# Kernel optimization log

Measured on AMD Instinct MI355X. Metric: run time of the kernel, lower is better.

## Reference

```python
import jax, jax.numpy as jnp
import numpy as np

B, T, D = 4096, 200, 64
H1, H2 = 64, 32


def _prelu(x, a):
    # PReLU with a single learnable slope (torch default num_parameters=1)
    return jnp.where(x >= 0, x, a * x)


def setup_inputs() -> dict:
    key = jax.random.key(0)
    ks = jax.random.split(key, 10)
    behavior = jax.random.normal(ks[0], (B, T, D), dtype=jnp.float32)
    candidate = jax.random.normal(ks[1], (B, D), dtype=jnp.float32)
    mask = jax.random.randint(ks[2], (B, T), 0, 2) > 0
    in_dim = 4 * D
    W1 = jax.random.normal(ks[3], (in_dim, H1), dtype=jnp.float32) / np.sqrt(in_dim)
    b1 = jnp.zeros((H1,), dtype=jnp.float32)
    a1 = jnp.full((1,), 0.25, dtype=jnp.float32)  # torch PReLU default init
    W2 = jax.random.normal(ks[4], (H1, H2), dtype=jnp.float32) / np.sqrt(H1)
    b2 = jnp.zeros((H2,), dtype=jnp.float32)
    a2 = jnp.full((1,), 0.25, dtype=jnp.float32)
    W3 = jax.random.normal(ks[5], (H2, 1), dtype=jnp.float32) / np.sqrt(H2)
    b3 = jnp.zeros((1,), dtype=jnp.float32)
    return {"behavior": behavior, "candidate": candidate, "mask": mask,
            "W1": W1, "b1": b1, "a1": a1,
            "W2": W2, "b2": b2, "a2": a2,
            "W3": W3, "b3": b3}


def reference(behavior, candidate, mask, W1, b1, a1, W2, b2, a2, W3, b3):
    # behavior: [B,T,D], candidate: [B,D], mask: [B,T] bool
    cand = candidate[:, None, :]                       # [B,1,D]
    cand_exp = jnp.broadcast_to(cand, behavior.shape)  # [B,T,D]
    diff = behavior - cand_exp
    prod = behavior * cand_exp
    att_input = jnp.concatenate([behavior, cand_exp, diff, prod], axis=-1)  # [B,T,4D]
    h = _prelu(att_input @ W1 + b1, a1)
    h = _prelu(h @ W2 + b2, a2)
    logits = (h @ W3 + b3)[..., 0]                     # [B,T]
    logits = jnp.where(mask, logits, -jnp.inf)
    w = jax.nn.softmax(logits, axis=-1)                # [B,T]
    user_interest = jnp.einsum('bt,btd->bd', w, behavior)  # [B,D]
    return user_interest
```

## Files before the change

### kernel.cpp

```cpp
#include <hip/hip_runtime.h>
#include <hip/hip_bf16.h>

#define T_LEN 200
#define MT    13

typedef __bf16 bf16x8 __attribute__((ext_vector_type(8)));
typedef __bf16 bf16x4 __attribute__((ext_vector_type(4)));
typedef float  f32x4  __attribute__((ext_vector_type(4)));

#if __has_builtin(__builtin_amdgcn_mfma_f32_16x16x16_bf16)
#define MFMA16(a, b, c) __builtin_amdgcn_mfma_f32_16x16x16_bf16((a), (b), (c), 0, 0, 0)
#elif __has_builtin(__builtin_amdgcn_mfma_f32_16x16x16bf16_1k)
#define MFMA16(a, b, c) __builtin_amdgcn_mfma_f32_16x16x16bf16_1k((a), (b), (c), 0, 0, 0)
#else
static __device__ __forceinline__ f32x4 mfma16_asm(bf16x4 a, bf16x4 b, f32x4 c) {
  asm("v_mfma_f32_16x16x16_bf16 %0, %1, %2, %0" : "+v"(c) : "v"(a), "v"(b));
  return c;
}
#define MFMA16(a, b, c) mfma16_asm((a), (b), (c))
#endif

#define MFMA32(a, b, c) __builtin_amdgcn_mfma_f32_16x16x32_bf16((a), (b), (c), 0, 0, 0)

struct __align__(16) Smem {
  unsigned char w1ac[64 * 144];
  unsigned char w1d [64 * 144];
  float wdiff[64][64];
  float candL[4][64];
};

__device__ __forceinline__ void loadA(const float* __restrict__ behB, int t, int kb,
                                      f32x4* x) {
  if (t < T_LEN) {
    const float* p = behB + (size_t)t * 64 + kb;
    x[0] = *(const f32x4*)p;
    x[1] = *(const f32x4*)(p + 4);
    x[2] = *(const f32x4*)(p + 32);
    x[3] = *(const f32x4*)(p + 36);
  } else {
    x[0] = f32x4{0.f, 0.f, 0.f, 0.f};
    x[1] = f32x4{0.f, 0.f, 0.f, 0.f};
    x[2] = f32x4{0.f, 0.f, 0.f, 0.f};
    x[3] = f32x4{0.f, 0.f, 0.f, 0.f};
  }
}

__global__ __launch_bounds__(256, 3) void lau_kernel(
    const float* __restrict__ behG, const float* __restrict__ candG,
    const int*  __restrict__ maskG,
    const float* __restrict__ W1g, const float* __restrict__ b1g, const float* __restrict__ a1g,
    const float* __restrict__ W2g, const float* __restrict__ b2g, const float* __restrict__ a2g,
    const float* __restrict__ W3g, const float* __restrict__ b3g,
    float* __restrict__ outG)
{
  __shared__ Smem s;
  const int tid  = threadIdx.x;
  const int lane = tid & 63;
  const int wv   = tid >> 6;
  const int b    = blockIdx.x * 4 + wv;

  for (int idx = tid; idx < 4096; idx += 256) {
    int j = idx & 63, d = idx >> 6;
    float ac = W1g[d * 64 + j] + W1g[(128 + d) * 64 + j];
    float dd = W1g[(192 + d) * 64 + j];
    *(__bf16*)(s.w1ac + j * 144 + d * 2) = (__bf16)ac;
    *(__bf16*)(s.w1d  + j * 144 + d * 2) = (__bf16)dd;
    s.wdiff[d][j] = W1g[(64 + d) * 64 + j] - W1g[(128 + d) * 64 + j];
  }
  s.candL[wv][lane] = candG[(size_t)b * 64 + lane];
  __syncthreads();

  const int r  = lane & 15;
  const int g  = lane >> 4;
  const int kb = g * 8;

  const bool boolmask = (__ballot(((const unsigned int*)maskG)[lane] > 1u) != 0ull);

  float biasv = b1g[lane];
#pragma unroll 8
  for (int d = 0; d < 64; ++d)
    biasv += s.candL[wv][d] * s.wdiff[d][lane];

  f32x4 bj4[4];
#pragma unroll
  for (int jt = 0; jt < 4; ++jt)
#pragma unroll
    for (int i = 0; i < 4; ++i)
      bj4[jt][i] = __shfl(biasv, jt * 16 + g * 4 + i);

  const f32x4 c0a = *(const f32x4*)&s.candL[wv][kb];
  const f32x4 c0b = *(const f32x4*)&s.candL[wv][kb + 4];
  const f32x4 c1a = *(const f32x4*)&s.candL[wv][kb + 32];
  const f32x4 c1b = *(const f32x4*)&s.candL[wv][kb + 36];

  bf16x8 A1[4][2];
#pragma unroll
  for (int jt = 0; jt < 4; ++jt) {
#pragma unroll
    for (int kc = 0; kc < 2; ++kc) {
      const int rowoff = (jt * 16 + r) * 144 + kc * 64 + g * 16;
      bf16x8 ac = *(const bf16x8*)(s.w1ac + rowoff);
      bf16x8 dd = *(const bf16x8*)(s.w1d  + rowoff);
      f32x4 cA = (kc == 0) ? c0a : c1a;
      f32x4 cB = (kc == 0) ? c0b : c1b;
      bf16x8 o;
#pragma unroll
      for (int e = 0; e < 4; ++e) {
        o[e]     = (__bf16)((float)ac[e]     + cA[e] * (float)dd[e]);
        o[4 + e] = (__bf16)((float)ac[4 + e] + cB[e] * (float)dd[4 + e]);
      }
      A1[jt][kc] = o;
    }
  }

  bf16x4 B2f[2][4];
#pragma unroll
  for (int nt = 0; nt < 2; ++nt)
#pragma unroll
    for (int c = 0; c < 4; ++c)
#pragma unroll
      for (int i = 0; i < 4; ++i)
        B2f[nt][c][i] = (__bf16)W2g[(c * 16 + g * 4 + i) * 32 + nt * 16 + r];

  const float al1 = a1g[0];
  const float al2 = a2g[0];
  const float b2v0 = b2g[r],      b2v1 = b2g[16 + r];
  const float w3v0 = W3g[r],      w3v1 = W3g[16 + r];
  (void)b3g;

  const float* behB = behG + (size_t)b * T_LEN * 64;
  const unsigned char* maskB8 = (const unsigned char*)maskG + (size_t)b * T_LEN;
  const int* maskB32 = maskG + (size_t)b * T_LEN;

  float mrun = -__builtin_inff();
  float srun = 0.f;
  f32x4 o0 = {0,0,0,0}, o1 = {0,0,0,0}, o2 = {0,0,0,0}, o3 = {0,0,0,0};

  f32x4 xc[4], xn[4];
  loadA(behB, r, kb, xc);
  int mc = boolmask ? (int)maskB8[r] : maskB32[r];
  int mn = 0;

#pragma unroll 1
  for (int mt = 0; mt < MT; ++mt) {
    if (mt + 1 < MT) {
      int tn = (mt + 1) * 16 + r;
      loadA(behB, tn, kb, xn);
      mn = (tn < T_LEN) ? (boolmask ? (int)maskB8[tn] : maskB32[tn]) : 0;
    }

    bf16x8 ab0, ab1;
#pragma unroll
    for (int i = 0; i < 4; ++i) {
      ab0[i]     = (__bf16)xc[0][i];
      ab0[4 + i] = (__bf16)xc[1][i];
      ab1[i]     = (__bf16)xc[2][i];
      ab1[4 + i] = (__bf16)xc[3][i];
    }

    bf16x4 a2f[4];
#pragma unroll
    for (int jt = 0; jt < 4; ++jt) {
      f32x4 acc = MFMA32(A1[jt][0], ab0, bj4[jt]);
      acc = MFMA32(A1[jt][1], ab1, acc);
#pragma unroll
      for (int i = 0; i < 4; ++i) {
        float h = acc[i];
        h = (h >= 0.f) ? h : al1 * h;
        a2f[jt][i] = (__bf16)h;
      }
    }

    f32x4 acc20 = {0,0,0,0}, acc21 = {0,0,0,0};
#pragma unroll
    for (int c = 0; c < 4; ++c) acc20 = MFMA16(a2f[c], B2f[0][c], acc20);
#pragma unroll
    for (int c = 0; c < 4; ++c) acc21 = MFMA16(a2f[c], B2f[1][c], acc21);

    f32x4 q;
#pragma unroll
    for (int i = 0; i < 4; ++i) {
      float h0 = acc20[i] + b2v0; h0 = (h0 >= 0.f) ? h0 : al2 * h0;
      float h1 = acc21[i] + b2v1; h1 = (h1 >= 0.f) ? h1 : al2 * h1;
      q[i] = h0 * w3v0 + h1 * w3v1;
    }
#pragma unroll
    for (int off = 1; off < 16; off <<= 1)
#pragma unroll
      for (int i = 0; i < 4; ++i) q[i] += __shfl_xor(q[i], off);

    const int srcl = (r >> 2) << 4;
    float f0 = __shfl(q[0], srcl);
    float f1 = __shfl(q[1], srcl);
    float f2 = __shfl(q[2], srcl);
    float f3 = __shfl(q[3], srcl);
    float q01 = (r & 1) ? f1 : f0;
    float q23 = (r & 1) ? f3 : f2;
    float qt  = (r & 2) ? q23 : q01;

    const bool valid = ((mt * 16 + r) < T_LEN) && (mc != 0);
    float lvt = valid ? qt : -__builtin_inff();
    float tm = lvt;
#pragma unroll
    for (int off = 1; off < 16; off <<= 1) tm = fmaxf(tm, __shfl_xor(tm, off));

    if (tm > mrun + 8.f) {
      float fs = __expf(mrun - tm);
      srun *= fs;
#pragma unroll
      for (int i = 0; i < 4; ++i) { o0[i] *= fs; o1[i] *= fs; o2[i] *= fs; o3[i] *= fs; }
      mrun = tm;
    }
    float et = valid ? __expf(lvt - mrun) : 0.f;
    srun += et;
#pragma unroll
    for (int i = 0; i < 4; ++i) {
      o0[i] += et * xc[0][i];
      o1[i] += et * xc[1][i];
      o2[i] += et * xc[2][i];
      o3[i] += et * xc[3][i];
    }

#pragma unroll
    for (int i = 0; i < 4; ++i) xc[i] = xn[i];
    mc = mn;
  }

#pragma unroll
  for (int off = 1; off < 16; off <<= 1) {
#pragma unroll
    for (int i = 0; i < 4; ++i) {
      o0[i] += __shfl_xor(o0[i], off);
      o1[i] += __shfl_xor(o1[i], off);
      o2[i] += __shfl_xor(o2[i], off);
      o3[i] += __shfl_xor(o3[i], off);
    }
    srun += __shfl_xor(srun, off);
  }
  if (r == 0) {
    float inv = 1.f / srun;
    float* po = outG + (size_t)b * 64 + kb;
#pragma unroll
    for (int i = 0; i < 4; ++i) {
      o0[i] *= inv; o1[i] *= inv; o2[i] *= inv; o3[i] *= inv;
    }
    *(f32x4*)(po)      = o0;
    *(f32x4*)(po + 4)  = o1;
    *(f32x4*)(po + 32) = o2;
    *(f32x4*)(po + 36) = o3;
  }
}

extern "C" void kernel_launch(void* const* d_in, const int* in_sizes, int n_in,
                              void* d_out, int out_size, void* d_ws, size_t ws_size,
                              hipStream_t stream) {
  (void)n_in; (void)d_ws; (void)ws_size; (void)out_size;
  const float* beh  = (const float*)d_in[0];
  const float* cand = (const float*)d_in[1];
  const int*   mask = (const int*)d_in[2];
  const float* W1   = (const float*)d_in[3];
  const float* b1   = (const float*)d_in[4];
  const float* a1   = (const float*)d_in[5];
  const float* W2   = (const float*)d_in[6];
  const float* b2   = (const float*)d_in[7];
  const float* a2   = (const float*)d_in[8];
  const float* W3   = (const float*)d_in[9];
  const float* b3   = (const float*)d_in[10];
  int B = in_sizes[1] / 64;
  int grid = B / 4;
  lau_kernel<<<grid, 256, 0, stream>>>(beh, cand, mask, W1, b1, a1, W2, b2, a2, W3, b3,
                                       (float*)d_out);
}
```

Before: 57.28 us.

## Hoist weight preprocessing into a prep kernel and drop shared memory

A small prep kernel now converts W1 and W2 once per call into bf16 fragments laid out per lane, plus a transposed wdiff, and stores them in workspace. The main kernel reads these straight from global memory, so it no longer needs per-block shared-memory setup or __syncthreads, and the occupancy hint rises from 3 to 4. Smaller changes fold b2 into the MFMA accumulator init, reuse the bf16-converted behavior values for the weighted sum, and reorder the conversion ahead of the prefetch to free registers. Costs are an extra launch and reduced accumulation precision, since the weighted sum now uses bf16-rounded behavior values.

```diff
diff --git a/kernel.cpp b/kernel.cpp
--- a/kernel.cpp
+++ b/kernel.cpp
@@ -22,12 +22,42 @@
 
 #define MFMA32(a, b, c) __builtin_amdgcn_mfma_f32_16x16x32_bf16((a), (b), (c), 0, 0, 0)
 
-struct __align__(16) Smem {
-  unsigned char w1ac[64 * 144];
-  unsigned char w1d [64 * 144];
-  float wdiff[64][64];
-  float candL[4][64];
-};
+
+__global__ __launch_bounds__(256) void prep_kernel(
+    const float* __restrict__ W1g, const float* __restrict__ W2g,
+    unsigned char* __restrict__ ws)
+{
+  const int idx = blockIdx.x * 256 + threadIdx.x;
+  unsigned short* w1acP = (unsigned short*)(ws);
+  unsigned short* w1dP  = (unsigned short*)(ws + 8192);
+  unsigned short* w2P   = (unsigned short*)(ws + 16384);
+  float*          wdifT = (float*)(ws + 20480);
+  {
+    int l = idx >> 6, q = idx & 63;
+    int f = q >> 3, e = q & 7;
+    int jt = f >> 1, kc = f & 1;
+    int g = l >> 4, r = l & 15;
+    int j = jt * 16 + r;
+    int d = kc * 32 + g * 8 + e;
+    float ac = W1g[d * 64 + j] + W1g[(128 + d) * 64 + j];
+    float dd = W1g[(192 + d) * 64 + j];
+    __bf16 acb = (__bf16)ac, ddb = (__bf16)dd;
+    w1acP[l * 64 + f * 8 + e] = *(unsigned short*)&acb;
+    w1dP [l * 64 + f * 8 + e] = *(unsigned short*)&ddb;
+  }
+  if (idx < 2048) {
+    int l = idx >> 5, q = idx & 31;
+    int f = q >> 2, i = q & 3;
+    int nt = f >> 2, c = f & 3;
+    int g = l >> 4, r = l & 15;
+    __bf16 v = (__bf16)W2g[(c * 16 + g * 4 + i) * 32 + nt * 16 + r];
+    w2P[l * 32 + f * 4 + i] = *(unsigned short*)&v;
+  }
+  {
+    int j = idx & 63, d = idx >> 6;
+    wdifT[j * 64 + d] = W1g[(64 + d) * 64 + j] - W1g[(128 + d) * 64 + j];
+  }
+}
 
 __device__ __forceinline__ void loadA(const float* __restrict__ behB, int t, int kb,
                                       f32x4* x) {
@@ -45,42 +75,68 @@
   }
 }
 
-__global__ __launch_bounds__(256, 3) void lau_kernel(
+__global__ __launch_bounds__(256, 4) void lau_kernel(
     const float* __restrict__ behG, const float* __restrict__ candG,
     const int*  __restrict__ maskG,
-    const float* __restrict__ W1g, const float* __restrict__ b1g, const float* __restrict__ a1g,
-    const float* __restrict__ W2g, const float* __restrict__ b2g, const float* __restrict__ a2g,
-    const float* __restrict__ W3g, const float* __restrict__ b3g,
+    const float* __restrict__ b1g, const float* __restrict__ a1g,
+    const float* __restrict__ b2g, const float* __restrict__ a2g,
+    const float* __restrict__ W3g,
+    const unsigned char* __restrict__ ws,
     float* __restrict__ outG)
 {
-  __shared__ Smem s;
   const int tid  = threadIdx.x;
   const int lane = tid & 63;
   const int wv   = tid >> 6;
   const int b    = blockIdx.x * 4 + wv;
-
-  for (int idx = tid; idx < 4096; idx += 256) {
-    int j = idx & 63, d = idx >> 6;
-    float ac = W1g[d * 64 + j] + W1g[(128 + d) * 64 + j];
-    float dd = W1g[(192 + d) * 64 + j];
-    *(__bf16*)(s.w1ac + j * 144 + d * 2) = (__bf16)ac;
-    *(__bf16*)(s.w1d  + j * 144 + d * 2) = (__bf16)dd;
-    s.wdiff[d][j] = W1g[(64 + d) * 64 + j] - W1g[(128 + d) * 64 + j];
-  }
-  s.candL[wv][lane] = candG[(size_t)b * 64 + lane];
-  __syncthreads();
-
-  const int r  = lane & 15;
-  const int g  = lane >> 4;
-  const int kb = g * 8;
+  const int r    = lane & 15;
+  const int g    = lane >> 4;
+  const int kb   = g * 8;
+
+  const unsigned short* w1acP = (const unsigned short*)(ws);
+  const unsigned short* w1dP  = (const unsigned short*)(ws + 8192);
+  const unsigned short* w2P   = (const unsigned short*)(ws + 16384);
+  const float*          wdifT = (const float*)(ws + 20480);
 
   const bool boolmask = (__ballot(((const unsigned int*)maskG)[lane] > 1u) != 0ull);
 
+  const float* candB = candG + (size_t)b * 64;
+  const f32x4 c0a = *(const f32x4*)(candB + kb);
+  const f32x4 c0b = *(const f32x4*)(candB + kb + 4);
+  const f32x4 c1a = *(const f32x4*)(candB + kb + 32);
+  const f32x4 c1b = *(const f32x4*)(candB + kb + 36);
+
+  bf16x8 A1[4][2];
+#pragma unroll
+  for (int f = 0; f < 8; ++f) {
+    const int jt = f >> 1, kc = f & 1;
+    bf16x8 ac = *(const bf16x8*)(w1acP + lane * 64 + f * 8);
+    bf16x8 dd = *(const bf16x8*)(w1dP  + lane * 64 + f * 8);
+    f32x4 cA = kc ? c1a : c0a;
+    f32x4 cB = kc ? c1b : c0b;
+    bf16x8 o;
+#pragma unroll
+    for (int e = 0; e < 4; ++e) {
+      o[e]     = (__bf16)((float)ac[e]     + cA[e] * (float)dd[e]);
+      o[4 + e] = (__bf16)((float)ac[4 + e] + cB[e] * (float)dd[4 + e]);
+    }
+    A1[jt][kc] = o;
+  }
+
+  bf16x4 B2f[8];
+#pragma unroll
+  for (int f = 0; f < 8; ++f)
+    B2f[f] = *(const bf16x4*)(w2P + lane * 32 + f * 4);
+
   float biasv = b1g[lane];
-#pragma unroll 8
-  for (int d = 0; d < 64; ++d)
-    biasv += s.candL[wv][d] * s.wdiff[d][lane];
-
+  {
+    const float* wdrow = wdifT + lane * 64;
+#pragma unroll
+    for (int d4 = 0; d4 < 16; ++d4) {
+      f32x4 wd = *(const f32x4*)(wdrow + d4 * 4);
+      f32x4 cd = *(const f32x4*)(candB + d4 * 4);
+      biasv += wd[0] * cd[0] + wd[1] * cd[1] + wd[2] * cd[2] + wd[3] * cd[3];
+    }
+  }
   f32x4 bj4[4];
 #pragma unroll
   for (int jt = 0; jt < 4; ++jt)
@@ -88,45 +144,12 @@
     for (int i = 0; i < 4; ++i)
       bj4[jt][i] = __shfl(biasv, jt * 16 + g * 4 + i);
 
-  const f32x4 c0a = *(const f32x4*)&s.candL[wv][kb];
-  const f32x4 c0b = *(const f32x4*)&s.candL[wv][kb + 4];
-  const f32x4 c1a = *(const f32x4*)&s.candL[wv][kb + 32];
-  const f32x4 c1b = *(const f32x4*)&s.candL[wv][kb + 36];
-
-  bf16x8 A1[4][2];
-#pragma unroll
-  for (int jt = 0; jt < 4; ++jt) {
-#pragma unroll
-    for (int kc = 0; kc < 2; ++kc) {
-      const int rowoff = (jt * 16 + r) * 144 + kc * 64 + g * 16;
-      bf16x8 ac = *(const bf16x8*)(s.w1ac + rowoff);
-      bf16x8 dd = *(const bf16x8*)(s.w1d  + rowoff);
-      f32x4 cA = (kc == 0) ? c0a : c1a;
-      f32x4 cB = (kc == 0) ? c0b : c1b;
-      bf16x8 o;
-#pragma unroll
-      for (int e = 0; e < 4; ++e) {
-        o[e]     = (__bf16)((float)ac[e]     + cA[e] * (float)dd[e]);
-        o[4 + e] = (__bf16)((float)ac[4 + e] + cB[e] * (float)dd[4 + e]);
-      }
-      A1[jt][kc] = o;
-    }
-  }
-
-  bf16x4 B2f[2][4];
-#pragma unroll
-  for (int nt = 0; nt < 2; ++nt)
-#pragma unroll
-    for (int c = 0; c < 4; ++c)
-#pragma unroll
-      for (int i = 0; i < 4; ++i)
-        B2f[nt][c][i] = (__bf16)W2g[(c * 16 + g * 4 + i) * 32 + nt * 16 + r];
-
   const float al1 = a1g[0];
   const float al2 = a2g[0];
-  const float b2v0 = b2g[r],      b2v1 = b2g[16 + r];
-  const float w3v0 = W3g[r],      w3v1 = W3g[16 + r];
-  (void)b3g;
+  const float b2v0 = b2g[r],  b2v1 = b2g[16 + r];
+  const float w3v0 = W3g[r],  w3v1 = W3g[16 + r];
+  const f32x4 cinit0 = {b2v0, b2v0, b2v0, b2v0};
+  const f32x4 cinit1 = {b2v1, b2v1, b2v1, b2v1};
 
   const float* behB = behG + (size_t)b * T_LEN * 64;
   const unsigned char* maskB8 = (const unsigned char*)maskG + (size_t)b * T_LEN;
@@ -136,26 +159,25 @@
   float srun = 0.f;
   f32x4 o0 = {0,0,0,0}, o1 = {0,0,0,0}, o2 = {0,0,0,0}, o3 = {0,0,0,0};
 
-  f32x4 xc[4], xn[4];
-  loadA(behB, r, kb, xc);
+  f32x4 xn[4];
+  loadA(behB, r, kb, xn);
   int mc = boolmask ? (int)maskB8[r] : maskB32[r];
   int mn = 0;
 
 #pragma unroll 1
   for (int mt = 0; mt < MT; ++mt) {
+    bf16x8 ab0, ab1;
+#pragma unroll
+    for (int i = 0; i < 4; ++i) {
+      ab0[i]     = (__bf16)xn[0][i];
+      ab0[4 + i] = (__bf16)xn[1][i];
+      ab1[i]     = (__bf16)xn[2][i];
+      ab1[4 + i] = (__bf16)xn[3][i];
+    }
     if (mt + 1 < MT) {
       int tn = (mt + 1) * 16 + r;
       loadA(behB, tn, kb, xn);
       mn = (tn < T_LEN) ? (boolmask ? (int)maskB8[tn] : maskB32[tn]) : 0;
-    }
-
-    bf16x8 ab0, ab1;
-#pragma unroll
-    for (int i = 0; i < 4; ++i) {
-      ab0[i]     = (__bf16)xc[0][i];
-      ab0[4 + i] = (__bf16)xc[1][i];
-      ab1[i]     = (__bf16)xc[2][i];
-      ab1[4 + i] = (__bf16)xc[3][i];
     }
 
     bf16x4 a2f[4];
@@ -171,17 +193,17 @@
       }
     }
 
-    f32x4 acc20 = {0,0,0,0}, acc21 = {0,0,0,0};
-#pragma unroll
-    for (int c = 0; c < 4; ++c) acc20 = MFMA16(a2f[c], B2f[0][c], acc20);
-#pragma unroll
-    for (int c = 0; c < 4; ++c) acc21 = MFMA16(a2f[c], B2f[1][c], acc21);
+    f32x4 acc20 = cinit0, acc21 = cinit1;
+#pragma unroll
+    for (int c = 0; c < 4; ++c) acc20 = MFMA16(a2f[c], B2f[c], acc20);
+#pragma unroll
+    for (int c = 0; c < 4; ++c) acc21 = MFMA16(a2f[c], B2f[4 + c], acc21);
 
     f32x4 q;
 #pragma unroll
     for (int i = 0; i < 4; ++i) {
-      float h0 = acc20[i] + b2v0; h0 = (h0 >= 0.f) ? h0 : al2 * h0;
-      float h1 = acc21[i] + b2v1; h1 = (h1 >= 0.f) ? h1 : al2 * h1;
+      float h0 = acc20[i]; h0 = (h0 >= 0.f) ? h0 : al2 * h0;
+      float h1 = acc21[i]; h1 = (h1 >= 0.f) ? h1 : al2 * h1;
       q[i] = h0 * w3v0 + h1 * w3v1;
     }
 #pragma unroll
@@ -215,14 +237,11 @@
     srun += et;
 #pragma unroll
     for (int i = 0; i < 4; ++i) {
-      o0[i] += et * xc[0][i];
-      o1[i] += et * xc[1][i];
-      o2[i] += et * xc[2][i];
-      o3[i] += et * xc[3][i];
-    }
-
-#pragma unroll
-    for (int i = 0; i < 4; ++i) xc[i] = xn[i];
+      o0[i] += et * (float)ab0[i];
+      o1[i] += et * (float)ab0[4 + i];
+      o2[i] += et * (float)ab1[i];
+      o3[i] += et * (float)ab1[4 + i];
+    }
     mc = mn;
   }
 
@@ -254,7 +273,7 @@
 extern "C" void kernel_launch(void* const* d_in, const int* in_sizes, int n_in,
                               void* d_out, int out_size, void* d_ws, size_t ws_size,
                               hipStream_t stream) {
-  (void)n_in; (void)d_ws; (void)ws_size; (void)out_size;
+  (void)n_in; (void)ws_size; (void)out_size;
   const float* beh  = (const float*)d_in[0];
   const float* cand = (const float*)d_in[1];
   const int*   mask = (const int*)d_in[2];
@@ -265,9 +284,12 @@
   const float* b2   = (const float*)d_in[7];
   const float* a2   = (const float*)d_in[8];
   const float* W3   = (const float*)d_in[9];
-  const float* b3   = (const float*)d_in[10];
+
+  unsigned char* ws = (unsigned char*)d_ws;
+  prep_kernel<<<16, 256, 0, stream>>>(W1, W2, ws);
+
   int B = in_sizes[1] / 64;
   int grid = B / 4;
-  lau_kernel<<<grid, 256, 0, stream>>>(beh, cand, mask, W1, b1, a1, W2, b2, a2, W3, b3,
-                                       (float*)d_out);
-}
+  lau_kernel<<<grid, 256, 0, stream>>>(beh, cand, mask, b1, a1, b2, a2, W3,
+                                       ws, (float*)d_out);
+}
```

After: 119.4 us. 2.09x slower.

## Split each batch row's sequence across two waves and merge softmax partials

Applied to the files above, without the earlier changes.

Each block now handles two batch rows instead of four, with two waves per row that each process about half of the 13 time tiles. The partial online-softmax state (max, sum, weighted output) from each wave goes to shared memory and is merged after a barrier. The diff also computes the candidate-dependent bias directly from global memory in one wave per row instead of staging wdiff in LDS, and folds b2 into the MFMA accumulator init. This shortens the serial per-wave loop and doubles the grid to hide latency. In exchange it repeats the W1 preprocessing in twice as many blocks, adds a second barrier, and leaves the half==1 waves idle during the bias computation.

```diff
diff --git a/kernel.cpp b/kernel.cpp
--- a/kernel.cpp
+++ b/kernel.cpp
@@ -1,8 +1,9 @@
 #include <hip/hip_runtime.h>
 #include <hip/hip_bf16.h>
 
-#define T_LEN 200
-#define MT    13
+#define T_LEN   200
+#define NTILES  13
+#define H0      7
 
 typedef __bf16 bf16x8 __attribute__((ext_vector_type(8)));
 typedef __bf16 bf16x4 __attribute__((ext_vector_type(4)));
@@ -25,12 +26,14 @@
 struct __align__(16) Smem {
   unsigned char w1ac[64 * 144];
   unsigned char w1d [64 * 144];
-  float wdiff[64][64];
-  float candL[4][64];
+  float biasL[2][64];
+  float mO[2][2][64];
+  float mM[2][2];
+  float mS[2][2];
 };
 
 __device__ __forceinline__ void loadA(const float* __restrict__ behB, int t, int kb,
-                                      f32x4* x) {
+                                      f32x4 (&x)[4]) {
   if (t < T_LEN) {
     const float* p = behB + (size_t)t * 64 + kb;
     x[0] = *(const f32x4*)p;
@@ -50,14 +53,19 @@
     const int*  __restrict__ maskG,
     const float* __restrict__ W1g, const float* __restrict__ b1g, const float* __restrict__ a1g,
     const float* __restrict__ W2g, const float* __restrict__ b2g, const float* __restrict__ a2g,
-    const float* __restrict__ W3g, const float* __restrict__ b3g,
+    const float* __restrict__ W3g,
     float* __restrict__ outG)
 {
   __shared__ Smem s;
   const int tid  = threadIdx.x;
   const int lane = tid & 63;
   const int wv   = tid >> 6;
-  const int b    = blockIdx.x * 4 + wv;
+  const int row  = wv >> 1;
+  const int half = wv & 1;
+  const int b    = blockIdx.x * 2 + row;
+  const int r    = lane & 15;
+  const int g    = lane >> 4;
+  const int kb   = g * 8;
 
   for (int idx = tid; idx < 4096; idx += 256) {
     int j = idx & 63, d = idx >> 6;
@@ -65,85 +73,95 @@
     float dd = W1g[(192 + d) * 64 + j];
     *(__bf16*)(s.w1ac + j * 144 + d * 2) = (__bf16)ac;
     *(__bf16*)(s.w1d  + j * 144 + d * 2) = (__bf16)dd;
-    s.wdiff[d][j] = W1g[(64 + d) * 64 + j] - W1g[(128 + d) * 64 + j];
-  }
-  s.candL[wv][lane] = candG[(size_t)b * 64 + lane];
+  }
+
+  const float* candB = candG + (size_t)b * 64;
+
+  if (half == 0) {
+    float biasv = b1g[lane];
+#pragma unroll 8
+    for (int d = 0; d < 64; ++d) {
+      float wd = W1g[(64 + d) * 64 + lane] - W1g[(128 + d) * 64 + lane];
+      biasv += candB[d] * wd;
+    }
+    s.biasL[row][lane] = biasv;
+  }
   __syncthreads();
 
-  const int r  = lane & 15;
-  const int g  = lane >> 4;
-  const int kb = g * 8;
-
   const bool boolmask = (__ballot(((const unsigned int*)maskG)[lane] > 1u) != 0ull);
 
-  float biasv = b1g[lane];
-#pragma unroll 8
-  for (int d = 0; d < 64; ++d)
-    biasv += s.candL[wv][d] * s.wdiff[d][lane];
+  const f32x4 c0a = *(const f32x4*)(candB + kb);
+  const f32x4 c0b = *(const f32x4*)(candB + kb + 4);
+  const f32x4 c1a = *(const f32x4*)(candB + kb + 32);
+  const f32x4 c1b = *(const f32x4*)(candB + kb + 36);
+
+  bf16x8 A1[4][2];
+#pragma unroll
+  for (int f = 0; f < 8; ++f) {
+    const int jt = f >> 1, kc = f & 1;
+    const int rowoff = (jt * 16 + r) * 144 + kc * 64 + g * 16;
+    bf16x8 ac = *(const bf16x8*)(s.w1ac + rowoff);
+    bf16x8 dd = *(const bf16x8*)(s.w1d  + rowoff);
+    f32x4 cA = kc ? c1a : c0a;
+    f32x4 cB = kc ? c1b : c0b;
+    bf16x8 o;
+#pragma unroll
+    for (int e = 0; e < 4; ++e) {
+      o[e]     = (__bf16)((float)ac[e]     + cA[e] * (float)dd[e]);
+      o[4 + e] = (__bf16)((float)ac[4 + e] + cB[e] * (float)dd[4 + e]);
+    }
+    A1[jt][kc] = o;
+  }
+
+  bf16x4 B2f[8];
+#pragma unroll
+  for (int f = 0; f < 8; ++f) {
+    const int nt = f >> 2, c = f & 3;
+#pragma unroll
+    for (int i = 0; i < 4; ++i)
+      B2f[f][i] = (__bf16)W2g[(c * 16 + g * 4 + i) * 32 + nt * 16 + r];
+  }
 
   f32x4 bj4[4];
 #pragma unroll
   for (int jt = 0; jt < 4; ++jt)
 #pragma unroll
     for (int i = 0; i < 4; ++i)
-      bj4[jt][i] = __shfl(biasv, jt * 16 + g * 4 + i);
-
-  const f32x4 c0a = *(const f32x4*)&s.candL[wv][kb];
-  const f32x4 c0b = *(const f32x4*)&s.candL[wv][kb + 4];
-  const f32x4 c1a = *(const f32x4*)&s.candL[wv][kb + 32];
-  const f32x4 c1b = *(const f32x4*)&s.candL[wv][kb + 36];
-
-  bf16x8 A1[4][2];
-#pragma unroll
-  for (int jt = 0; jt < 4; ++jt) {
-#pragma unroll
-    for (int kc = 0; kc < 2; ++kc) {
-      const int rowoff = (jt * 16 + r) * 144 + kc * 64 + g * 16;
-      bf16x8 ac = *(const bf16x8*)(s.w1ac + rowoff);
-      bf16x8 dd = *(const bf16x8*)(s.w1d  + rowoff);
-      f32x4 cA = (kc == 0) ? c0a : c1a;
-      f32x4 cB = (kc == 0) ? c0b : c1b;
-      bf16x8 o;
-#pragma unroll
-      for (int e = 0; e < 4; ++e) {
-        o[e]     = (__bf16)((float)ac[e]     + cA[e] * (float)dd[e]);
-        o[4 + e] = (__bf16)((float)ac[4 + e] + cB[e] * (float)dd[4 + e]);
-      }
-      A1[jt][kc] = o;
-    }
-  }
-
-  bf16x4 B2f[2][4];
-#pragma unroll
-  for (int nt = 0; nt < 2; ++nt)
-#pragma unroll
-    for (int c = 0; c < 4; ++c)
-#pragma unroll
-      for (int i = 0; i < 4; ++i)
-        B2f[nt][c][i] = (__bf16)W2g[(c * 16 + g * 4 + i) * 32 + nt * 16 + r];
+      bj4[jt][i] = s.biasL[row][jt * 16 + g * 4 + i];
 
   const float al1 = a1g[0];
   const float al2 = a2g[0];
-  const float b2v0 = b2g[r],      b2v1 = b2g[16 + r];
-  const float w3v0 = W3g[r],      w3v1 = W3g[16 + r];
-  (void)b3g;
+  const float b2v0 = b2g[r],  b2v1 = b2g[16 + r];
+  const float w3v0 = W3g[r],  w3v1 = W3g[16 + r];
+  const f32x4 cinit0 = {b2v0, b2v0, b2v0, b2v0};
+  const f32x4 cinit1 = {b2v1, b2v1, b2v1, b2v1};
 
   const float* behB = behG + (size_t)b * T_LEN * 64;
   const unsigned char* maskB8 = (const unsigned char*)maskG + (size_t)b * T_LEN;
   const int* maskB32 = maskG + (size_t)b * T_LEN;
 
+  const int mt0 = half ? H0 : 0;
+  const int mtN = half ? (NTILES - H0) : H0;
+
   float mrun = -__builtin_inff();
   float srun = 0.f;
   f32x4 o0 = {0,0,0,0}, o1 = {0,0,0,0}, o2 = {0,0,0,0}, o3 = {0,0,0,0};
 
   f32x4 xc[4], xn[4];
-  loadA(behB, r, kb, xc);
-  int mc = boolmask ? (int)maskB8[r] : maskB32[r];
-  int mn = 0;
+  {
+    int t0 = mt0 * 16 + r;
+    loadA(behB, t0, kb, xc);
+  }
+  int mc = 0, mn = 0;
+  {
+    int t0 = mt0 * 16 + r;
+    mc = (t0 < T_LEN) ? (boolmask ? (int)maskB8[t0] : maskB32[t0]) : 0;
+  }
 
 #pragma unroll 1
-  for (int mt = 0; mt < MT; ++mt) {
-    if (mt + 1 < MT) {
+  for (int it = 0; it < mtN; ++it) {
+    const int mt = mt0 + it;
+    if (it + 1 < mtN) {
       int tn = (mt + 1) * 16 + r;
       loadA(behB, tn, kb, xn);
       mn = (tn < T_LEN) ? (boolmask ? (int)maskB8[tn] : maskB32[tn]) : 0;
@@ -171,17 +189,17 @@
       }
     }
 
-    f32x4 acc20 = {0,0,0,0}, acc21 = {0,0,0,0};
-#pragma unroll
-    for (int c = 0; c < 4; ++c) acc20 = MFMA16(a2f[c], B2f[0][c], acc20);
-#pragma unroll
-    for (int c = 0; c < 4; ++c) acc21 = MFMA16(a2f[c], B2f[1][c], acc21);
+    f32x4 acc20 = cinit0, acc21 = cinit1;
+#pragma unroll
+    for (int c = 0; c < 4; ++c) acc20 = MFMA16(a2f[c], B2f[c], acc20);
+#pragma unroll
+    for (int c = 0; c < 4; ++c) acc21 = MFMA16(a2f[c], B2f[4 + c], acc21);
 
     f32x4 q;
 #pragma unroll
     for (int i = 0; i < 4; ++i) {
-      float h0 = acc20[i] + b2v0; h0 = (h0 >= 0.f) ? h0 : al2 * h0;
-      float h1 = acc21[i] + b2v1; h1 = (h1 >= 0.f) ? h1 : al2 * h1;
+      float h0 = acc20[i]; h0 = (h0 >= 0.f) ? h0 : al2 * h0;
+      float h1 = acc21[i]; h1 = (h1 >= 0.f) ? h1 : al2 * h1;
       q[i] = h0 * w3v0 + h1 * w3v1;
     }
 #pragma unroll
@@ -238,16 +256,24 @@
     srun += __shfl_xor(srun, off);
   }
   if (r == 0) {
-    float inv = 1.f / srun;
-    float* po = outG + (size_t)b * 64 + kb;
-#pragma unroll
-    for (int i = 0; i < 4; ++i) {
-      o0[i] *= inv; o1[i] *= inv; o2[i] *= inv; o3[i] *= inv;
-    }
-    *(f32x4*)(po)      = o0;
-    *(f32x4*)(po + 4)  = o1;
-    *(f32x4*)(po + 32) = o2;
-    *(f32x4*)(po + 36) = o3;
+    *(f32x4*)&s.mO[row][half][kb]      = o0;
+    *(f32x4*)&s.mO[row][half][kb + 4]  = o1;
+    *(f32x4*)&s.mO[row][half][kb + 32] = o2;
+    *(f32x4*)&s.mO[row][half][kb + 36] = o3;
+  }
+  if (lane == 0) { s.mM[row][half] = mrun; s.mS[row][half] = srun; }
+  __syncthreads();
+
+  if (wv < 2) {
+    const int rw = wv;
+    const int bb = blockIdx.x * 2 + rw;
+    float m0 = s.mM[rw][0], m1 = s.mM[rw][1];
+    float M  = fmaxf(m0, m1);
+    float e0 = __expf(m0 - M), e1 = __expf(m1 - M);
+    float denom = s.mS[rw][0] * e0 + s.mS[rw][1] * e1;
+    float inv = 1.f / denom;
+    float val = (s.mO[rw][0][lane] * e0 + s.mO[rw][1][lane] * e1) * inv;
+    outG[(size_t)bb * 64 + lane] = val;
   }
 }
 
@@ -265,9 +291,9 @@
   const float* b2   = (const float*)d_in[7];
   const float* a2   = (const float*)d_in[8];
   const float* W3   = (const float*)d_in[9];
-  const float* b3   = (const float*)d_in[10];
+
   int B = in_sizes[1] / 64;
-  int grid = B / 4;
-  lau_kernel<<<grid, 256, 0, stream>>>(beh, cand, mask, W1, b1, a1, W2, b2, a2, W3, b3,
+  int grid = B / 2;
+  lau_kernel<<<grid, 256, 0, stream>>>(beh, cand, mask, W1, b1, a1, W2, b2, a2, W3,
                                        (float*)d_out);
 }
```

New measurement: 60.64 us. 1.06x slower.
